# Kernel optimization log

Measured on AMD Instinct MI355X. Metric: run time of the kernel, lower is better.

The kernel has to match this reference:

```python
import jax, jax.numpy as jnp
import numpy as np

LN_EPS = 1e-5      # torch nn.LayerNorm default
NORM_EPS = 1e-12   # torch F.normalize default
EPS = 1e-8         # loss eps


def layer_norm(x, gamma, beta):
    mu = x.mean(axis=-1, keepdims=True)
    var = x.var(axis=-1, keepdims=True)  # biased, matches torch LN
    return (x - mu) * jax.lax.rsqrt(var + LN_EPS) * gamma + beta


def l2norm(x):
    n = jnp.sqrt(jnp.sum(x * x, axis=-1, keepdims=True))
    return x / jnp.maximum(n, NORM_EPS)


def setup_inputs() -> dict:
    key = jax.random.key(0)
    k1, k2, k3 = jax.random.split(key, 3)
    N, B, L, D = 1024, 64, 197, 768
    text_features = jax.random.normal(k1, (N, D), dtype=jnp.float32)
    vision_tokens = jax.random.normal(k2, (B, L, D), dtype=jnp.float32)
    group_map = jnp.sort(jax.random.randint(k3, (N,), 0, B)).astype(jnp.int64)
    ln_gamma = jnp.ones((D,), dtype=jnp.float32)
    ln_beta = jnp.zeros((D,), dtype=jnp.float32)
    log_loss_temp = jnp.array([np.log(0.07)], dtype=jnp.float32)
    return {
        "text_features": text_features,
        "vision_tokens": vision_tokens,
        "group_map": group_map,
        "ln_gamma": ln_gamma,
        "ln_beta": ln_beta,
        "log_loss_temp": log_loss_temp,
    }


def reference(text_features, vision_tokens, group_map, ln_gamma, ln_beta, log_loss_temp):
    D = text_features.shape[-1]
    # shared LayerNorm on both modalities
    tf = layer_norm(text_features, ln_gamma, ln_beta)          # [N, D]
    vt = layer_norm(vision_tokens, ln_gamma, ln_beta)          # [B, L, D]

    # SimilarityLogit, sim_op='dot': scores / sqrt(D), softmax over tokens
    scores = jnp.einsum('nd,bld->bnl', tf, vt) / jnp.sqrt(jnp.float32(D))
    attn = jax.nn.softmax(scores, axis=-1)                     # [B, N, L]
    aggregated = jnp.einsum('bnl,bld->bnd', attn, vt)          # [B, N, D]

    qn = l2norm(tf)                                            # [N, D]
    an = l2norm(aggregated)                                    # [B, N, D]
    logits = jnp.einsum('nd,bnd->nb', qn, an)                  # [N, B] (== [B,N].T)

    # multi-positive NCE loss (row_sum=False, col_sum=False)
    temp = jnp.exp(log_loss_temp)[0]
    scaled = jnp.exp(logits / temp)                            # [N, B]
    N = scaled.shape[0]
    idx = jnp.arange(N)
    pos = scaled[idx, group_map]                               # [N]

    # row loss: pos / sum over images
    row_p = pos / (scaled.sum(axis=1) + EPS)
    row_loss = -jnp.log(row_p + EPS)

    # column loss: pos / (pos + sum of negatives in its column)
    neg_mask = jnp.ones_like(scaled).at[idx, group_map].set(0.0)
    sum_neg = (scaled * neg_mask).sum(axis=0)[group_map]       # [N]
    col_p = pos / (pos + sum_neg + EPS)
    col_loss = -jnp.log(col_p + EPS)

    return (row_loss.mean() + col_loss.mean()) / 2
```

## Files before the change

### kernel.cpp

```cpp
#include <hip/hip_runtime.h>
#include <hip/hip_bf16.h>
#include <math.h>

#define NN 1024
#define BB 64
#define LL 197
#define LP 256
#define DD 768

typedef __attribute__((ext_vector_type(8))) short short8;
typedef __attribute__((ext_vector_type(4))) float f32x4;

constexpr float LN_EPS = 1e-5f;
constexpr float NORM_EPS = 1e-12f;
constexpr float EPS = 1e-8f;

__device__ __forceinline__ float waveSum(float v) {
#pragma unroll
    for (int m = 32; m >= 1; m >>= 1) v += __shfl_xor(v, m, 64);
    return v;
}
__device__ __forceinline__ float grpSum(float v) {
#pragma unroll
    for (int m = 8; m >= 1; m >>= 1) v += __shfl_xor(v, m, 64);
    return v;
}
__device__ __forceinline__ float grpMax(float v) {
#pragma unroll
    for (int m = 8; m >= 1; m >>= 1) v = fmaxf(v, __shfl_xor(v, m, 64));
    return v;
}

__device__ __forceinline__ float bf2f(unsigned short u) {
    unsigned int x = ((unsigned int)u) << 16;
    return reinterpret_cast<float&>(x);
}

__device__ __forceinline__ void gl_lds16(const void* g, void* l) {
    __builtin_amdgcn_global_load_lds(
        (const __attribute__((address_space(1))) unsigned int*)g,
        (__attribute__((address_space(3))) unsigned int*)l, 16, 0, 0);
}

__global__ __launch_bounds__(256) void ln_kernel(
    const float* __restrict__ x, __hip_bfloat16* __restrict__ y,
    const float* __restrict__ gamma, const float* __restrict__ beta,
    float* __restrict__ qinv) {
    const int row = blockIdx.x;
    const int tid = threadIdx.x;
    const float* xr = x + (size_t)row * DD;
    __hip_bfloat16* yr = y + (size_t)row * DD;

    float v[3];
    float s = 0.f, ss = 0.f;
#pragma unroll
    for (int c = 0; c < 3; c++) {
        float t = xr[tid + 256 * c];
        v[c] = t; s += t; ss += t * t;
    }
    __shared__ float red[8];
    s = waveSum(s); ss = waveSum(ss);
    const int w = tid >> 6;
    if ((tid & 63) == 0) { red[w] = s; red[4 + w] = ss; }
    __syncthreads();
    s = red[0] + red[1] + red[2] + red[3];
    ss = red[4] + red[5] + red[6] + red[7];
    const float mean = s * (1.f / DD);
    const float var = ss * (1.f / DD) - mean * mean;
    const float rs = rsqrtf(var + LN_EPS);

    float q = 0.f;
#pragma unroll
    for (int c = 0; c < 3; c++) {
        const int d = tid + 256 * c;
        float t = (v[c] - mean) * rs * gamma[d] + beta[d];
        __hip_bfloat16 hb = __float2bfloat16(t);
        yr[d] = hb;
        float tb = __bfloat162float(hb);
        q += tb * tb;
    }
    __syncthreads();
    q = waveSum(q);
    if ((tid & 63) == 0) red[w] = q;
    __syncthreads();
    if (tid == 0) {
        float n2 = red[0] + red[1] + red[2] + red[3];
        qinv[row] = 1.f / fmaxf(sqrtf(n2), NORM_EPS);
    }
}

__global__ __launch_bounds__(256) void ln_vis_kernel(
    const float* __restrict__ x, __hip_bfloat16* __restrict__ y,
    const float* __restrict__ gamma, const float* __restrict__ beta) {
    const int id = blockIdx.x;
    const int xcd = id & 7;
    const int k = id >> 3;
    const int bhi = k >> 8;
    const int l = k & 255;
    const int b = xcd + 8 * bhi;
    const int tid = threadIdx.x;
    __hip_bfloat16* yr = y + ((size_t)b * LP + l) * DD;
    if (l >= LL) {
#pragma unroll
        for (int c = 0; c < 3; c++) yr[tid + 256 * c] = __float2bfloat16(0.f);
        return;
    }
    const float* xr = x + ((size_t)b * LL + l) * DD;

    float v[3];
    float s = 0.f, ss = 0.f;
#pragma unroll
    for (int c = 0; c < 3; c++) {
        float t = xr[tid + 256 * c];
        v[c] = t; s += t; ss += t * t;
    }
    __shared__ float red[8];
    s = waveSum(s); ss = waveSum(ss);
    const int w = tid >> 6;
    if ((tid & 63) == 0) { red[w] = s; red[4 + w] = ss; }
    __syncthreads();
    s = red[0] + red[1] + red[2] + red[3];
    ss = red[4] + red[5] + red[6] + red[7];
    const float mean = s * (1.f / DD);
    const float var = ss * (1.f / DD) - mean * mean;
    const float rs = rsqrtf(var + LN_EPS);
#pragma unroll
    for (int c = 0; c < 3; c++) {
        const int d = tid + 256 * c;
        yr[d] = __float2bfloat16((v[c] - mean) * rs * gamma[d] + beta[d]);
    }
}

__global__ __launch_bounds__(256, 4) void gram_kernel(
    const __hip_bfloat16* __restrict__ vt, __hip_bfloat16* __restrict__ G) {
    const int id = blockIdx.x;
    const int xcd = id & 7;
    const int k = id >> 3;
    const int bhi = k >> 3;
    const int rb = k & 7;
    const int b = xcd + 8 * bhi;
    const int n0 = rb * 32;
    const int tid = threadIdx.x, w = tid >> 6, lane = tid & 63;
    const int g = lane >> 4, c = lane & 15;
    const int gsw = (g ^ ((c ^ (c >> 2)) & 3)) * 16;

    __shared__ __align__(16) unsigned char smem[36864];
    const char* vtbc = (const char*)(vt + (size_t)b * LP * DD);

#define GSTAGE(ks, bsel)                                                        \
    {                                                                           \
        const int kb_ = (ks) * 64;                                              \
        _Pragma("unroll")                                                       \
        for (int q_ = 0; q_ < 4; q_++) {                                        \
            const int o_ = q_ * 4096 + tid * 16;                                \
            const int r_ = o_ >> 6;                                             \
            const int sj_ = ((o_ >> 4) & 3) ^ ((r_ ^ (r_ >> 2)) & 3);           \
            gl_lds16(vtbc + (size_t)r_ * 1536 + kb_ + sj_ * 16,                 \
                     smem + (bsel) * 16384 + q_ * 4096 + w * 1024);             \
        }                                                                       \
        if (w < 2) {                                                            \
            const int o_ = tid * 16;                                            \
            const int r_ = o_ >> 6;                                             \
            const int sj_ = ((o_ >> 4) & 3) ^ ((r_ ^ (r_ >> 2)) & 3);           \
            gl_lds16(vtbc + (size_t)(n0 + r_) * 1536 + kb_ + sj_ * 16,          \
                     smem + 32768 + (bsel) * 2048 + w * 1024);                  \
        }                                                                       \
    }

    f32x4 acc[4][2];
#pragma unroll
    for (int i = 0; i < 4; i++)
#pragma unroll
        for (int nb = 0; nb < 2; nb++) acc[i][nb] = {0.f, 0.f, 0.f, 0.f};

    GSTAGE(0, 0);
    asm volatile("s_waitcnt vmcnt(0)" ::: "memory");
    __syncthreads();

    for (int ks = 0; ks < 24; ks++) {
        const int cur = ks & 1;
        if (ks < 23) GSTAGE(ks + 1, cur ^ 1);
        const unsigned char* vb = smem + cur * 16384;
        const unsigned char* tb = smem + 32768 + cur * 2048;
        short8 af[2], bf[4];
#pragma unroll
        for (int nb = 0; nb < 2; nb++)
            af[nb] = *(const short8*)(tb + (nb * 16 + c) * 64 + gsw);
#pragma unroll
        for (int i = 0; i < 4; i++)
            bf[i] = *(const short8*)(vb + ((w + 4 * i) * 16 + c) * 64 + gsw);
#pragma unroll
        for (int i = 0; i < 4; i++)
#pragma unroll
            for (int nb = 0; nb < 2; nb++)
                acc[i][nb] = __builtin_amdgcn_mfma_f32_16x16x32_bf16(
                    af[nb], bf[i], acc[i][nb], 0, 0, 0);
        asm volatile("s_waitcnt vmcnt(0)" ::: "memory");
        __syncthreads();
    }
#undef GSTAGE

    __hip_bfloat16* Gb = G + (size_t)b * LP * LP;
#pragma unroll
    for (int i = 0; i < 4; i++) {
        const int col = (w + 4 * i) * 16 + c;
#pragma unroll
        for (int nb = 0; nb < 2; nb++)
#pragma unroll
            for (int r = 0; r < 4; r++)
                Gb[(size_t)(n0 + nb * 16 + g * 4 + r) * LP + col] =
                    __float2bfloat16(acc[i][nb][r]);
    }
}

__global__ __launch_bounds__(256, 3) void score_kernel(
    const __hip_bfloat16* __restrict__ tf, const __hip_bfloat16* __restrict__ vt,
    const float* __restrict__ qinv, __hip_bfloat16* __restrict__ Pbuf,
    float* __restrict__ numq) {
    const int id = blockIdx.x;
    const int xcd = id & 7;
    const int kk = id >> 3;
    const int bhi = kk >> 4;
    const int nt = kk & 15;
    const int b = xcd + 8 * bhi;
    const int n0 = nt * 64;
    const int tid = threadIdx.x, w = tid >> 6, lane = tid & 63;
    const int g = lane >> 4, c = lane & 15;
    const int gsw = (g ^ ((c ^ (c >> 2)) & 3)) * 16;

    __shared__ __align__(16) unsigned char smem[40960];
    float* mx = (float*)smem;
    float* sm = mx + 256;
    float* nm = sm + 256;

    const char* vtbc = (const char*)(vt + (size_t)b * LP * DD);
    const char* tfc = (const char*)(tf + (size_t)n0 * DD);

#define SSTAGE(ks, bsel)                                                        \
    {                                                                           \
        const int kb_ = (ks) * 64;                                              \
        _Pragma("unroll")                                                       \
        for (int q_ = 0; q_ < 4; q_++) {                                        \
            const int o_ = q_ * 4096 + tid * 16;                                \
            const int r_ = o_ >> 6;                                             \
            const int sj_ = ((o_ >> 4) & 3) ^ ((r_ ^ (r_ >> 2)) & 3);           \
            gl_lds16(vtbc + (size_t)r_ * 1536 + kb_ + sj_ * 16,                 \
                     smem + (bsel) * 16384 + q_ * 4096 + w * 1024);             \
        }                                                                       \
        {                                                                       \
            const int o_ = tid * 16;                                            \
            const int r_ = o_ >> 6;                                             \
            const int sj_ = ((o_ >> 4) & 3) ^ ((r_ ^ (r_ >> 2)) & 3);           \
            gl_lds16(tfc + (size_t)r_ * 1536 + kb_ + sj_ * 16,                  \
                     smem + 32768 + (bsel) * 4096 + w * 1024);                  \
        }                                                                       \
    }

    f32x4 acc[4][4];
#pragma unroll
    for (int i = 0; i < 4; i++)
#pragma unroll
        for (int nb = 0; nb < 4; nb++) acc[i][nb] = {0.f, 0.f, 0.f, 0.f};

    SSTAGE(0, 0);
    asm volatile("s_waitcnt vmcnt(0)" ::: "memory");
    __syncthreads();

    for (int ks = 0; ks < 24; ks++) {
        const int cur = ks & 1;
        if (ks < 23) SSTAGE(ks + 1, cur ^ 1);
        const unsigned char* vb = smem + cur * 16384;
        const unsigned char* tb = smem + 32768 + cur * 4096;
        short8 af[4], bf[4];
#pragma unroll
        for (int nb = 0; nb < 4; nb++)
            af[nb] = *(const short8*)(tb + (nb * 16 + c) * 64 + gsw);
#pragma unroll
        for (int i = 0; i < 4; i++)
            bf[i] = *(const short8*)(vb + ((w + 4 * i) * 16 + c) * 64 + gsw);
#pragma unroll
        for (int i = 0; i < 4; i++)
#pragma unroll
            for (int nb = 0; nb < 4; nb++)
                acc[i][nb] = __builtin_amdgcn_mfma_f32_16x16x32_bf16(
                    af[nb], bf[i], acc[i][nb], 0, 0, 0);
        asm volatile("s_waitcnt vmcnt(0)" ::: "memory");
        __syncthreads();
    }
#undef SSTAGE

    const float inv_sqrtD = 0.0360843918f;
    float mp[4][4];
#pragma unroll
    for (int nb = 0; nb < 4; nb++)
#pragma unroll
        for (int r = 0; r < 4; r++) mp[nb][r] = -1e30f;
#pragma unroll
    for (int i = 0; i < 4; i++) {
        const int l = (w + 4 * i) * 16 + c;
        if (l < LL) {
#pragma unroll
            for (int nb = 0; nb < 4; nb++)
#pragma unroll
                for (int r = 0; r < 4; r++) mp[nb][r] = fmaxf(mp[nb][r], acc[i][nb][r]);
        }
    }
#pragma unroll
    for (int nb = 0; nb < 4; nb++)
#pragma unroll
        for (int r = 0; r < 4; r++) mp[nb][r] = grpMax(mp[nb][r]);
    if (c == 0) {
#pragma unroll
        for (int nb = 0; nb < 4; nb++)
#pragma unroll
            for (int r = 0; r < 4; r++) mx[(nb * 16 + g * 4 + r) * 4 + w] = mp[nb][r];
    }
    __syncthreads();
    float mf[4][4];
#pragma unroll
    for (int nb = 0; nb < 4; nb++)
#pragma unroll
        for (int r = 0; r < 4; r++) {
            const int row = nb * 16 + g * 4 + r;
            mf[nb][r] = fmaxf(fmaxf(mx[row * 4 + 0], mx[row * 4 + 1]),
                              fmaxf(mx[row * 4 + 2], mx[row * 4 + 3]));
        }

    float sp[4][4], np[4][4];
#pragma unroll
    for (int nb = 0; nb < 4; nb++)
#pragma unroll
        for (int r = 0; r < 4; r++) { sp[nb][r] = 0.f; np[nb][r] = 0.f; }
#pragma unroll
    for (int i = 0; i < 4; i++) {
        const int l = (w + 4 * i) * 16 + c;
#pragma unroll
        for (int nb = 0; nb < 4; nb++)
#pragma unroll
            for (int r = 0; r < 4; r++) {
                const float raw = acc[i][nb][r];
                const float p = (l < LL) ? __expf((raw - mf[nb][r]) * inv_sqrtD) : 0.f;
                acc[i][nb][r] = p;
                sp[nb][r] += p;
                np[nb][r] += p * raw;
            }
    }
#pragma unroll
    for (int nb = 0; nb < 4; nb++)
#pragma unroll
        for (int r = 0; r < 4; r++) { sp[nb][r] = grpSum(sp[nb][r]); np[nb][r] = grpSum(np[nb][r]); }
    if (c == 0) {
#pragma unroll
        for (int nb = 0; nb < 4; nb++)
#pragma unroll
            for (int r = 0; r < 4; r++) {
                const int row = nb * 16 + g * 4 + r;
                sm[row * 4 + w] = sp[nb][r];
                nm[row * 4 + w] = np[nb][r];
            }
    }
    __syncthreads();

    float invs[4][4];
#pragma unroll
    for (int nb = 0; nb < 4; nb++)
#pragma unroll
        for (int r = 0; r < 4; r++) {
            const int row = nb * 16 + g * 4 + r;
            const float ssum = sm[row * 4 + 0] + sm[row * 4 + 1] + sm[row * 4 + 2] + sm[row * 4 + 3];
            invs[nb][r] = 1.f / ssum;
        }

    __hip_bfloat16* Pb = Pbuf + ((size_t)b * NN + n0) * LP;
#pragma unroll
    for (int i = 0; i < 4; i++) {
        const int lb = w + 4 * i;
#pragma unroll
        for (int nb = 0; nb < 4; nb++)
#pragma unroll
            for (int r = 0; r < 4; r++)
                Pb[(size_t)(nb * 16 + g * 4 + r) * LP + lb * 16 + c] =
                    __float2bfloat16(acc[i][nb][r] * invs[nb][r]);
    }

    if (tid < 64) {
        const int row = tid;
        const int n = n0 + row;
        const float ssum = sm[row * 4 + 0] + sm[row * 4 + 1] + sm[row * 4 + 2] + sm[row * 4 + 3];
        const float nsum = nm[row * 4 + 0] + nm[row * 4 + 1] + nm[row * 4 + 2] + nm[row * 4 + 3];
        numq[(size_t)n * BB + b] = (nsum / ssum) * qinv[n];
    }
}

__global__ __launch_bounds__(256, 3) void den_kernel(
    const __hip_bfloat16* __restrict__ Pbuf, const __hip_bfloat16* __restrict__ G,
    const float* __restrict__ numq, float* __restrict__ logits) {
    const int id = blockIdx.x;
    const int xcd = id & 7;
    const int kk = id >> 3;
    const int bhi = kk >> 4;
    const int nt = kk & 15;
    const int b = xcd + 8 * bhi;
    const int n0 = nt * 64;
    const int tid = threadIdx.x, w = tid >> 6, lane = tid & 63;
    const int g = lane >> 4, c = lane & 15;
    const int gsw = (g ^ ((c ^ (c >> 2)) & 3)) * 16;

    __shared__ __align__(16) unsigned char smem[40960];
    float* mx = (float*)smem;

    const char* Gbc = (const char*)(G + (size_t)b * LP * LP);
    const char* Pbc = (const char*)(Pbuf + ((size_t)b * NN + n0) * LP);

#define DSTAGE(ks, bsel)                                                        \
    {                                                                           \
        const int kb_ = (ks) * 64;                                              \
        _Pragma("unroll")                                                       \
        for (int q_ = 0; q_ < 4; q_++) {                                        \
            const int o_ = q_ * 4096 + tid * 16;                                \
            const int r_ = o_ >> 6;                                             \
            const int sj_ = ((o_ >> 4) & 3) ^ ((r_ ^ (r_ >> 2)) & 3);           \
            gl_lds16(Gbc + (size_t)r_ * 512 + kb_ + sj_ * 16,                   \
                     smem + (bsel) * 16384 + q_ * 4096 + w * 1024);             \
        }                                                                       \
        {                                                                       \
            const int o_ = tid * 16;                                            \
            const int r_ = o_ >> 6;                                             \
            const int sj_ = ((o_ >> 4) & 3) ^ ((r_ ^ (r_ >> 2)) & 3);           \
            gl_lds16(Pbc + (size_t)r_ * 512 + kb_ + sj_ * 16,                   \
                     smem + 32768 + (bsel) * 4096 + w * 1024);                  \
        }                                                                       \
    }

    f32x4 acc[4][4];
#pragma unroll
    for (int i = 0; i < 4; i++)
#pragma unroll
        for (int nb = 0; nb < 4; nb++) acc[i][nb] = {0.f, 0.f, 0.f, 0.f};

    DSTAGE(0, 0);
    asm volatile("s_waitcnt vmcnt(0)" ::: "memory");
    __syncthreads();

    for (int ks = 0; ks < 8; ks++) {
        const int cur = ks & 1;
        if (ks < 7) DSTAGE(ks + 1, cur ^ 1);
        const unsigned char* vb = smem + cur * 16384;
        const unsigned char* tb = smem + 32768 + cur * 4096;
        short8 af[4], bf[4];
#pragma unroll
        for (int nb = 0; nb < 4; nb++)
            af[nb] = *(const short8*)(tb + (nb * 16 + c) * 64 + gsw);
#pragma unroll
        for (int i = 0; i < 4; i++)
            bf[i] = *(const short8*)(vb + ((w + 4 * i) * 16 + c) * 64 + gsw);
#pragma unroll
        for (int i = 0; i < 4; i++)
#pragma unroll
            for (int nb = 0; nb < 4; nb++)
                acc[i][nb] = __builtin_amdgcn_mfma_f32_16x16x32_bf16(
                    af[nb], bf[i], acc[i][nb], 0, 0, 0);
        asm volatile("s_waitcnt vmcnt(0)" ::: "memory");
        __syncthreads();
    }
#undef DSTAGE

    const short* Pb = (const short*)Pbc;
    float den[4][4];
#pragma unroll
    for (int nb = 0; nb < 4; nb++)
#pragma unroll
        for (int r = 0; r < 4; r++) den[nb][r] = 0.f;
#pragma unroll
    for (int i = 0; i < 4; i++) {
        const int col = (w + 4 * i) * 16 + c;
#pragma unroll
        for (int nb = 0; nb < 4; nb++)
#pragma unroll
            for (int r = 0; r < 4; r++) {
                const float P = bf2f((unsigned short)Pb[(size_t)(nb * 16 + g * 4 + r) * LP + col]);
                den[nb][r] += P * acc[i][nb][r];
            }
    }

#pragma unroll
    for (int nb = 0; nb < 4; nb++)
#pragma unroll
        for (int r = 0; r < 4; r++) den[nb][r] = grpSum(den[nb][r]);
    if (c == 0) {
#pragma unroll
        for (int nb = 0; nb < 4; nb++)
#pragma unroll
            for (int r = 0; r < 4; r++) mx[(nb * 16 + g * 4 + r) * 4 + w] = den[nb][r];
    }
    __syncthreads();
    if (tid < 64) {
        const int row = tid;
        const int n = n0 + row;
        const float dsum = mx[row * 4 + 0] + mx[row * 4 + 1] + mx[row * 4 + 2] + mx[row * 4 + 3];
        const float dn = fmaxf(sqrtf(fmaxf(dsum, 0.f)), NORM_EPS);
        logits[(size_t)n * BB + b] = numq[(size_t)n * BB + b] / dn;
    }
}

__global__ __launch_bounds__(64) void loss_row_kernel(
    const float* __restrict__ logits, const int* __restrict__ gm,
    const float* __restrict__ logtemp, float* __restrict__ scaled,
    float* __restrict__ posv, float* __restrict__ rowloss) {
    const int n = blockIdx.x;
    const int b = threadIdx.x;
    const float invtemp = 1.f / expf(logtemp[0]);
    const float e = expf(logits[(size_t)n * BB + b] * invtemp);
    scaled[(size_t)n * BB + b] = e;
    const float sum = waveSum(e);
    const int g = gm[n];
    const float pos = __shfl(e, g, 64);
    if (b == 0) {
        posv[n] = pos;
        rowloss[n] = -logf(pos / (sum + EPS) + EPS);
    }
}

__global__ __launch_bounds__(256) void colsum_kernel(
    const float* __restrict__ scaled, const int* __restrict__ gm,
    float* __restrict__ colsum, float* __restrict__ poscol) {
    const int b = blockIdx.x;
    const int tid = threadIdx.x;
    float s = 0.f, p = 0.f;
    for (int n = tid; n < NN; n += 256) {
        const float e = scaled[(size_t)n * BB + b];
        s += e;
        if (gm[n] == b) p += e;
    }
    s = waveSum(s); p = waveSum(p);
    __shared__ float red[8];
    const int w = tid >> 6;
    if ((tid & 63) == 0) { red[w] = s; red[4 + w] = p; }
    __syncthreads();
    if (tid == 0) {
        colsum[b] = red[0] + red[1] + red[2] + red[3];
        poscol[b] = red[4] + red[5] + red[6] + red[7];
    }
}

__global__ __launch_bounds__(1024) void final_kernel(
    const float* __restrict__ posv, const float* __restrict__ rowloss,
    const float* __restrict__ colsum, const float* __restrict__ poscol,
    const int* __restrict__ gm, float* __restrict__ out) {
    const int n = threadIdx.x;
    const int g = gm[n];
    const float pos = posv[n];
    const float sum_neg = colsum[g] - poscol[g];
    const float cl = -logf(pos / (pos + sum_neg + EPS) + EPS);
    float v = rowloss[n] + cl;
    v = waveSum(v);
    __shared__ float red[16];
    if ((n & 63) == 0) red[n >> 6] = v;
    __syncthreads();
    if (n == 0) {
        float s = 0.f;
#pragma unroll
        for (int i = 0; i < 16; i++) s += red[i];
        out[0] = s / (2.f * NN);
    }
}

extern "C" void kernel_launch(void* const* d_in, const int* in_sizes, int n_in,
                              void* d_out, int out_size, void* d_ws, size_t ws_size,
                              hipStream_t stream) {
    const float* text = (const float*)d_in[0];
    const float* vis = (const float*)d_in[1];
    const int* gm = (const int*)d_in[2];
    const float* gamma = (const float*)d_in[3];
    const float* beta = (const float*)d_in[4];
    const float* logtemp = (const float*)d_in[5];
    float* out = (float*)d_out;

    char* w = (char*)d_ws;
    __hip_bfloat16* tf = (__hip_bfloat16*)w;             w += (size_t)NN * DD * 2;
    __hip_bfloat16* vt = (__hip_bfloat16*)w;             w += (size_t)BB * LP * DD * 2;
    __hip_bfloat16* G  = (__hip_bfloat16*)w;             w += (size_t)BB * LP * LP * 2;
    __hip_bfloat16* Pbuf = (__hip_bfloat16*)w;           w += (size_t)BB * NN * LP * 2;
    float* qinv    = (float*)w;  w += (size_t)NN * 4;
    float* numq    = (float*)w;  w += (size_t)NN * BB * 4;
    float* logits  = (float*)w;  w += (size_t)NN * BB * 4;
    float* scaled  = (float*)w;  w += (size_t)NN * BB * 4;
    float* posv    = (float*)w;  w += (size_t)NN * 4;
    float* rowloss = (float*)w;  w += (size_t)NN * 4;
    float* colsum  = (float*)w;  w += (size_t)BB * 4;
    float* poscol  = (float*)w;  w += (size_t)BB * 4;

    ln_kernel<<<NN, 256, 0, stream>>>(text, tf, gamma, beta, qinv);
    ln_vis_kernel<<<BB * LP, 256, 0, stream>>>(vis, vt, gamma, beta);

    score_kernel<<<1024, 256, 0, stream>>>(tf, vt, qinv, Pbuf, numq);
    gram_kernel<<<512, 256, 0, stream>>>(vt, G);
    den_kernel<<<1024, 256, 0, stream>>>(Pbuf, G, numq, logits);

    loss_row_kernel<<<NN, 64, 0, stream>>>(logits, gm, logtemp, scaled, posv, rowloss);
    colsum_kernel<<<BB, 256, 0, stream>>>(scaled, gm, colsum, poscol);
    final_kernel<<<1, 1024, 0, stream>>>(posv, rowloss, colsum, poscol, gm, out);
}
```

Measured before the change: 123.8 us.

## Deepen global-to-LDS pipeline from double to triple buffering in three GEMM kernels

```diff
diff --git a/kernel.cpp b/kernel.cpp
--- a/kernel.cpp
+++ b/kernel.cpp
@@ -131,7 +131,7 @@
     }
 }
 
-__global__ __launch_bounds__(256, 4) void gram_kernel(
+__global__ __launch_bounds__(256, 2) void gram_kernel(
     const __hip_bfloat16* __restrict__ vt, __hip_bfloat16* __restrict__ G) {
     const int id = blockIdx.x;
     const int xcd = id & 7;
@@ -144,7 +144,7 @@
     const int g = lane >> 4, c = lane & 15;
     const int gsw = (g ^ ((c ^ (c >> 2)) & 3)) * 16;
 
-    __shared__ __align__(16) unsigned char smem[36864];
+    __shared__ __align__(16) unsigned char smem[55296];
     const char* vtbc = (const char*)(vt + (size_t)b * LP * DD);
 
 #define GSTAGE(ks, bsel)                                                        \
@@ -163,7 +163,7 @@
             const int r_ = o_ >> 6;                                             \
             const int sj_ = ((o_ >> 4) & 3) ^ ((r_ ^ (r_ >> 2)) & 3);           \
             gl_lds16(vtbc + (size_t)(n0 + r_) * 1536 + kb_ + sj_ * 16,          \
-                     smem + 32768 + (bsel) * 2048 + w * 1024);                  \
+                     smem + 49152 + (bsel) * 2048 + w * 1024);                  \
         }                                                                       \
     }
 
@@ -174,14 +174,14 @@
         for (int nb = 0; nb < 2; nb++) acc[i][nb] = {0.f, 0.f, 0.f, 0.f};
 
     GSTAGE(0, 0);
-    asm volatile("s_waitcnt vmcnt(0)" ::: "memory");
+    GSTAGE(1, 1);
+    asm volatile("s_waitcnt vmcnt(4)" ::: "memory");
     __syncthreads();
 
     for (int ks = 0; ks < 24; ks++) {
-        const int cur = ks & 1;
-        if (ks < 23) GSTAGE(ks + 1, cur ^ 1);
-        const unsigned char* vb = smem + cur * 16384;
-        const unsigned char* tb = smem + 32768 + cur * 2048;
+        if (ks < 22) GSTAGE(ks + 2, (ks + 2) % 3);
+        const unsigned char* vb = smem + (ks % 3) * 16384;
+        const unsigned char* tb = smem + 49152 + (ks % 3) * 2048;
         short8 af[2], bf[4];
 #pragma unroll
         for (int nb = 0; nb < 2; nb++)
@@ -195,7 +195,8 @@
             for (int nb = 0; nb < 2; nb++)
                 acc[i][nb] = __builtin_amdgcn_mfma_f32_16x16x32_bf16(
                     af[nb], bf[i], acc[i][nb], 0, 0, 0);
-        asm volatile("s_waitcnt vmcnt(0)" ::: "memory");
+        if (ks < 22) asm volatile("s_waitcnt vmcnt(4)" ::: "memory");
+        else         asm volatile("s_waitcnt vmcnt(0)" ::: "memory");
         __syncthreads();
     }
 #undef GSTAGE
@@ -228,7 +229,7 @@
     const int g = lane >> 4, c = lane & 15;
     const int gsw = (g ^ ((c ^ (c >> 2)) & 3)) * 16;
 
-    __shared__ __align__(16) unsigned char smem[40960];
+    __shared__ __align__(16) unsigned char smem[61440];
     float* mx = (float*)smem;
     float* sm = mx + 256;
     float* nm = sm + 256;
@@ -252,7 +253,7 @@
             const int r_ = o_ >> 6;                                             \
             const int sj_ = ((o_ >> 4) & 3) ^ ((r_ ^ (r_ >> 2)) & 3);           \
             gl_lds16(tfc + (size_t)r_ * 1536 + kb_ + sj_ * 16,                  \
-                     smem + 32768 + (bsel) * 4096 + w * 1024);                  \
+                     smem + 49152 + (bsel) * 4096 + w * 1024);                  \
         }                                                                       \
     }
 
@@ -263,14 +264,14 @@
         for (int nb = 0; nb < 4; nb++) acc[i][nb] = {0.f, 0.f, 0.f, 0.f};
 
     SSTAGE(0, 0);
-    asm volatile("s_waitcnt vmcnt(0)" ::: "memory");
+    SSTAGE(1, 1);
+    asm volatile("s_waitcnt vmcnt(5)" ::: "memory");
     __syncthreads();
 
     for (int ks = 0; ks < 24; ks++) {
-        const int cur = ks & 1;
-        if (ks < 23) SSTAGE(ks + 1, cur ^ 1);
-        const unsigned char* vb = smem + cur * 16384;
-        const unsigned char* tb = smem + 32768 + cur * 4096;
+        if (ks < 22) SSTAGE(ks + 2, (ks + 2) % 3);
+        const unsigned char* vb = smem + (ks % 3) * 16384;
+        const unsigned char* tb = smem + 49152 + (ks % 3) * 4096;
         short8 af[4], bf[4];
 #pragma unroll
         for (int nb = 0; nb < 4; nb++)
@@ -284,7 +285,8 @@
             for (int nb = 0; nb < 4; nb++)
                 acc[i][nb] = __builtin_amdgcn_mfma_f32_16x16x32_bf16(
                     af[nb], bf[i], acc[i][nb], 0, 0, 0);
-        asm volatile("s_waitcnt vmcnt(0)" ::: "memory");
+        if (ks < 22) asm volatile("s_waitcnt vmcnt(5)" ::: "memory");
+        else         asm volatile("s_waitcnt vmcnt(0)" ::: "memory");
         __syncthreads();
     }
 #undef SSTAGE
@@ -406,7 +408,7 @@
     const int g = lane >> 4, c = lane & 15;
     const int gsw = (g ^ ((c ^ (c >> 2)) & 3)) * 16;
 
-    __shared__ __align__(16) unsigned char smem[40960];
+    __shared__ __align__(16) unsigned char smem[61440];
     float* mx = (float*)smem;
 
     const char* Gbc = (const char*)(G + (size_t)b * LP * LP);
@@ -428,7 +430,7 @@
             const int r_ = o_ >> 6;                                             \
             const int sj_ = ((o_ >> 4) & 3) ^ ((r_ ^ (r_ >> 2)) & 3);           \
             gl_lds16(Pbc + (size_t)r_ * 512 + kb_ + sj_ * 16,                   \
-                     smem + 32768 + (bsel) * 4096 + w * 1024);                  \
+                     smem + 49152 + (bsel) * 4096 + w * 1024);                  \
         }                                                                       \
     }
 
@@ -439,14 +441,14 @@
         for (int nb = 0; nb < 4; nb++) acc[i][nb] = {0.f, 0.f, 0.f, 0.f};
 
     DSTAGE(0, 0);
-    asm volatile("s_waitcnt vmcnt(0)" ::: "memory");
+    DSTAGE(1, 1);
+    asm volatile("s_waitcnt vmcnt(5)" ::: "memory");
     __syncthreads();
 
     for (int ks = 0; ks < 8; ks++) {
-        const int cur = ks & 1;
-        if (ks < 7) DSTAGE(ks + 1, cur ^ 1);
-        const unsigned char* vb = smem + cur * 16384;
-        const unsigned char* tb = smem + 32768 + cur * 4096;
+        if (ks < 6) DSTAGE(ks + 2, (ks + 2) % 3);
+        const unsigned char* vb = smem + (ks % 3) * 16384;
+        const unsigned char* tb = smem + 49152 + (ks % 3) * 4096;
         short8 af[4], bf[4];
 #pragma unroll
         for (int nb = 0; nb < 4; nb++)
@@ -460,7 +462,8 @@
             for (int nb = 0; nb < 4; nb++)
                 acc[i][nb] = __builtin_amdgcn_mfma_f32_16x16x32_bf16(
                     af[nb], bf[i], acc[i][nb], 0, 0, 0);
-        asm volatile("s_waitcnt vmcnt(0)" ::: "memory");
+        if (ks < 6) asm volatile("s_waitcnt vmcnt(5)" ::: "memory");
+        else        asm volatile("s_waitcnt vmcnt(0)" ::: "memory");
         __syncthreads();
     }
 #undef DSTAGE
```

New measurement: 123.1 us. About the same (-0.5%).
